# Kernel optimization log

Hardware: AMD Instinct MI355X
Metric: run time of the kernel (lower is better)

The kernel has to match this reference:

```python
import jax, jax.numpy as jnp
import numpy as np

GRID = 128
N = GRID * GRID  # number of torus nodes, node id v = x + GRID * y
HID = 64
OUT = 1
BATCH = 64


def _neighbor_idx():
    # Replicates gen_neighbor_lists: sparse matrices are permutation gathers
    # (A x)[v] = x[neighbor(v)] on a periodic grid.
    idx = np.arange(N)
    xc = idx % GRID
    yc = idx // GRID
    up = xc + ((yc + 1) % GRID) * GRID
    down = xc + ((yc - 1) % GRID) * GRID
    left = (xc - 1) % GRID + yc * GRID
    right = (xc + 1) % GRID + yc * GRID
    return np.stack([up, down, left, right], axis=0).astype(np.int32)  # [4, N]

NBR = jnp.asarray(_neighbor_idx())


def setup_inputs() -> dict:
    key = jax.random.key(0)
    ks = jax.random.split(key, 7)
    s4, sh = 1.0 / np.sqrt(4.0), 1.0 / np.sqrt(HID)
    return {
        "x": jax.random.normal(ks[0], (BATCH, N, 2), dtype=jnp.float32),
        "H": jnp.eye(2, dtype=jnp.float32),
        "W_emb": jax.random.uniform(ks[1], (4, HID), jnp.float32, -s4, s4),
        "b_emb": jax.random.uniform(ks[2], (HID,), jnp.float32, -s4, s4),
        "W_hid": jax.random.uniform(ks[3], (HID, HID), jnp.float32, -sh, sh),
        "b_hid": jax.random.uniform(ks[4], (HID,), jnp.float32, -sh, sh),
        "W_post": jax.random.uniform(ks[5], (HID, OUT), jnp.float32, -sh, sh),
        "b_post": jax.random.uniform(ks[6], (OUT,), jnp.float32, -sh, sh),
    }


def reference(x, H, W_emb, b_emb, W_hid, b_hid, W_post, b_post):
    # Permutation-matrix sparse.mm == direct neighbor gather: [B, 4, N, 2]
    xn = x[:, NBR, :]
    # Bilinear form per direction/node: s[b,i,k] = sum_{m,n} x[b,i,m] H[m,n] xn[b,k,i,n]
    s = jnp.einsum('bim,bkin,mn->bik', x, xn, H)  # [B, N, 4]
    h = jax.nn.relu(s @ W_emb + b_emb)            # [B, N, HID]
    h = jax.nn.relu(h @ W_hid + b_hid)            # [B, N, HID]
    h = h @ W_post + b_post                       # [B, N, OUT]
    return h.sum(axis=1)                          # [B, OUT]
```

## Files before the change

### kernel.cpp

```cpp
#include <hip/hip_runtime.h>
#include <hip/hip_bf16.h>

#define GRID_D 128
#define NSITES (GRID_D * GRID_D)
#define HID 64
#define BATCH 64

#define WPB 4
#define BLOCKS 1024
#define BLOCKS_PER_BATCH (BLOCKS / BATCH)
#define WAVES_PER_BATCH (BLOCKS_PER_BATCH * WPB)
#define SITES_PER_WAVE (NSITES / WAVES_PER_BATCH)
#define ITERS (SITES_PER_WAVE / 64)

typedef short bf16x8 __attribute__((ext_vector_type(8)));
typedef float f32x4  __attribute__((ext_vector_type(4)));

__device__ __forceinline__ unsigned short f2bf(float f) {
    return __builtin_bit_cast(unsigned short, __float2bfloat16(f));
}

__device__ __forceinline__ unsigned cvt_pk_bf16(float a, float b) {
    unsigned r;
    asm("v_cvt_pk_bf16_f32 %0, %1, %2" : "=v"(r) : "v"(a), "v"(b));
    return r;
}

union frag_u { bf16x8 v; unsigned u[4]; unsigned short us[8]; };

__global__ __launch_bounds__(256)
void gauge_mfma(const float* __restrict__ x,
                const float* __restrict__ H,
                const float* __restrict__ W_emb,
                const float* __restrict__ b_emb,
                const float* __restrict__ W_hid,
                const float* __restrict__ b_hid,
                const float* __restrict__ W_post,
                float* __restrict__ ws)
{
    const int tid   = threadIdx.x;
    const int lane  = tid & 63;
    const int widx  = tid >> 6;
    const int wgid  = blockIdx.x * WPB + widx;
    const int b     = wgid / WAVES_PER_BATCH;
    const int wslot = wgid % WAVES_PER_BATCH;

    const int  ls  = lane & 15;
    const int  kg  = lane >> 4;
    const bool kg0 = (kg == 0);

    const float h00 = H[0], h01 = H[1], h10 = H[2], h11 = H[3];

    bf16x8 bfrag[4][2];
    #pragma unroll
    for (int t = 0; t < 4; ++t) {
        #pragma unroll
        for (int s = 0; s < 2; ++s) {
            frag_u r;
            #pragma unroll
            for (int j = 0; j < 4; ++j) {
                const int i    = 2 * j;
                const int khid = s * 32 + ((i & 4) << 2) + (kg << 2) + (i & 3);
                r.u[j] = cvt_pk_bf16(W_hid[khid * HID + t * 16 + ls],
                                     W_hid[(khid + 1) * HID + t * 16 + ls]);
            }
            bfrag[t][s] = r.v;
        }
    }

    bf16x8 afe[4];
    #pragma unroll
    for (int m = 0; m < 4; ++m) {
        const int col = m * 16 + ls;
        frag_u r;
        r.u[0] = kg0 ? cvt_pk_bf16(W_emb[0 * HID + col], W_emb[1 * HID + col]) : 0u;
        r.u[1] = kg0 ? cvt_pk_bf16(W_emb[2 * HID + col], W_emb[3 * HID + col]) : 0u;
        r.u[2] = kg0 ? (unsigned)f2bf(b_emb[col]) : 0u;
        r.u[3] = 0u;
        afe[m] = r.v;
    }

    float bh[4], wp[4];
    #pragma unroll
    for (int t = 0; t < 4; ++t) {
        bh[t] = b_hid[t * 16 + ls];
        wp[t] = W_post[t * 16 + ls];
    }

    const float* __restrict__ xb = x + (size_t)b * NSITES * 2;
    const int wbase = wslot * SITES_PER_WAVE;
    const unsigned sd2 = kg0 ? 0x00003F80u : 0u;
    float o0 = 0.f, o1 = 0.f, o2 = 0.f, o3 = 0.f;

    for (int it = 0; it < ITERS; ++it) {
        const int site = wbase + it * 64 + lane;
        const int xc = site & (GRID_D - 1);
        const int yc = site >> 7;
        const int n0 = xc + (((yc + 1) & (GRID_D - 1)) << 7);
        const int n1 = xc + (((yc - 1) & (GRID_D - 1)) << 7);
        const int n2 = ((xc - 1) & (GRID_D - 1)) + (yc << 7);
        const int n3 = ((xc + 1) & (GRID_D - 1)) + (yc << 7);

        const float2 xi = *(const float2*)(xb + 2 * site);
        const float2 xu = *(const float2*)(xb + 2 * n0);
        const float2 xd = *(const float2*)(xb + 2 * n1);
        const float2 xl = *(const float2*)(xb + 2 * n2);
        const float2 xr = *(const float2*)(xb + 2 * n3);

        const float s0 = xi.x * fmaf(h00, xu.x, h01 * xu.y) + xi.y * fmaf(h10, xu.x, h11 * xu.y);
        const float s1 = xi.x * fmaf(h00, xd.x, h01 * xd.y) + xi.y * fmaf(h10, xd.x, h11 * xd.y);
        const float s2 = xi.x * fmaf(h00, xl.x, h01 * xl.y) + xi.y * fmaf(h10, xl.x, h11 * xl.y);
        const float s3 = xi.x * fmaf(h00, xr.x, h01 * xr.y) + xi.y * fmaf(h10, xr.x, h11 * xr.y);

        const unsigned p01 = cvt_pk_bf16(s0, s1);
        const unsigned p23 = cvt_pk_bf16(s2, s3);

        #pragma unroll
        for (int g = 0; g < 4; ++g) {
            const unsigned q0 = __shfl(p01, (g << 4) + ls, 64);
            const unsigned q1 = __shfl(p23, (g << 4) + ls, 64);
            frag_u bs;
            bs.u[0] = kg0 ? q0 : 0u;
            bs.u[1] = kg0 ? q1 : 0u;
            bs.u[2] = sd2;
            bs.u[3] = 0u;

            f32x4 D0 = {0.f, 0.f, 0.f, 0.f};
            f32x4 D1 = {0.f, 0.f, 0.f, 0.f};
            f32x4 D2 = {0.f, 0.f, 0.f, 0.f};
            f32x4 D3 = {0.f, 0.f, 0.f, 0.f};
            D0 = __builtin_amdgcn_mfma_f32_16x16x32_bf16(afe[0], bs.v, D0, 0, 0, 0);
            D1 = __builtin_amdgcn_mfma_f32_16x16x32_bf16(afe[1], bs.v, D1, 0, 0, 0);
            D2 = __builtin_amdgcn_mfma_f32_16x16x32_bf16(afe[2], bs.v, D2, 0, 0, 0);
            D3 = __builtin_amdgcn_mfma_f32_16x16x32_bf16(afe[3], bs.v, D3, 0, 0, 0);

            #pragma unroll
            for (int r = 0; r < 4; ++r) {
                D0[r] = fmaxf(D0[r], 0.0f);
                D1[r] = fmaxf(D1[r], 0.0f);
                D2[r] = fmaxf(D2[r], 0.0f);
                D3[r] = fmaxf(D3[r], 0.0f);
            }
            frag_u ah0, ah1;
            ah0.u[0] = cvt_pk_bf16(D0[0], D0[1]);
            ah0.u[1] = cvt_pk_bf16(D0[2], D0[3]);
            ah0.u[2] = cvt_pk_bf16(D1[0], D1[1]);
            ah0.u[3] = cvt_pk_bf16(D1[2], D1[3]);
            ah1.u[0] = cvt_pk_bf16(D2[0], D2[1]);
            ah1.u[1] = cvt_pk_bf16(D2[2], D2[3]);
            ah1.u[2] = cvt_pk_bf16(D3[0], D3[1]);
            ah1.u[3] = cvt_pk_bf16(D3[2], D3[3]);

            {
                f32x4 acc = { bh[0], bh[0], bh[0], bh[0] };
                acc = __builtin_amdgcn_mfma_f32_16x16x32_bf16(ah0.v, bfrag[0][0], acc, 0, 0, 0);
                acc = __builtin_amdgcn_mfma_f32_16x16x32_bf16(ah1.v, bfrag[0][1], acc, 0, 0, 0);
                #pragma unroll
                for (int r = 0; r < 4; ++r) o0 = fmaf(fmaxf(acc[r], 0.0f), wp[0], o0);
            }
            {
                f32x4 acc = { bh[1], bh[1], bh[1], bh[1] };
                acc = __builtin_amdgcn_mfma_f32_16x16x32_bf16(ah0.v, bfrag[1][0], acc, 0, 0, 0);
                acc = __builtin_amdgcn_mfma_f32_16x16x32_bf16(ah1.v, bfrag[1][1], acc, 0, 0, 0);
                #pragma unroll
                for (int r = 0; r < 4; ++r) o1 = fmaf(fmaxf(acc[r], 0.0f), wp[1], o1);
            }
            {
                f32x4 acc = { bh[2], bh[2], bh[2], bh[2] };
                acc = __builtin_amdgcn_mfma_f32_16x16x32_bf16(ah0.v, bfrag[2][0], acc, 0, 0, 0);
                acc = __builtin_amdgcn_mfma_f32_16x16x32_bf16(ah1.v, bfrag[2][1], acc, 0, 0, 0);
                #pragma unroll
                for (int r = 0; r < 4; ++r) o2 = fmaf(fmaxf(acc[r], 0.0f), wp[2], o2);
            }
            {
                f32x4 acc = { bh[3], bh[3], bh[3], bh[3] };
                acc = __builtin_amdgcn_mfma_f32_16x16x32_bf16(ah0.v, bfrag[3][0], acc, 0, 0, 0);
                acc = __builtin_amdgcn_mfma_f32_16x16x32_bf16(ah1.v, bfrag[3][1], acc, 0, 0, 0);
                #pragma unroll
                for (int r = 0; r < 4; ++r) o3 = fmaf(fmaxf(acc[r], 0.0f), wp[3], o3);
            }
        }
    }

    float o = (o0 + o1) + (o2 + o3);

    #pragma unroll
    for (int off = 32; off > 0; off >>= 1)
        o += __shfl_down(o, off, 64);

    __shared__ float part[WPB];
    if (lane == 0) part[widx] = o;
    __syncthreads();
    if (tid == 0)
        ws[blockIdx.x] = part[0] + part[1] + part[2] + part[3];
}

__global__ __launch_bounds__(64)
void gauge_reduce(const float* __restrict__ ws,
                  const float* __restrict__ b_post,
                  float* __restrict__ out)
{
    const int b = threadIdx.x;
    float t = (float)NSITES * b_post[0];
    #pragma unroll
    for (int j = 0; j < BLOCKS_PER_BATCH; ++j)
        t += ws[b * BLOCKS_PER_BATCH + j];
    out[b] = t;
}

extern "C" void kernel_launch(void* const* d_in, const int* in_sizes, int n_in,
                              void* d_out, int out_size, void* d_ws, size_t ws_size,
                              hipStream_t stream)
{
    const float* x      = (const float*)d_in[0];
    const float* H      = (const float*)d_in[1];
    const float* W_emb  = (const float*)d_in[2];
    const float* b_emb  = (const float*)d_in[3];
    const float* W_hid  = (const float*)d_in[4];
    const float* b_hid  = (const float*)d_in[5];
    const float* W_post = (const float*)d_in[6];
    const float* b_post = (const float*)d_in[7];
    float* out = (float*)d_out;
    float* ws  = (float*)d_ws;

    gauge_mfma<<<dim3(BLOCKS), dim3(256), 0, stream>>>(
        x, H, W_emb, b_emb, W_hid, b_hid, W_post, ws);
    gauge_reduce<<<dim3(1), dim3(64), 0, stream>>>(ws, b_post, out);
}
```

Baseline: 92.89 us.

## Prefetch next iteration's bilinear inputs and fold reduction into atomics

```diff
diff --git a/kernel.cpp b/kernel.cpp
--- a/kernel.cpp
+++ b/kernel.cpp
@@ -36,7 +36,8 @@
                 const float* __restrict__ W_hid,
                 const float* __restrict__ b_hid,
                 const float* __restrict__ W_post,
-                float* __restrict__ ws)
+                const float* __restrict__ b_post,
+                float* __restrict__ out)
 {
     const int tid   = threadIdx.x;
     const int lane  = tid & 63;
@@ -92,7 +93,7 @@
     const unsigned sd2 = kg0 ? 0x00003F80u : 0u;
     float o0 = 0.f, o1 = 0.f, o2 = 0.f, o3 = 0.f;
 
-    for (int it = 0; it < ITERS; ++it) {
+    auto s_phase = [&](int it, unsigned& p01, unsigned& p23) {
         const int site = wbase + it * 64 + lane;
         const int xc = site & (GRID_D - 1);
         const int yc = site >> 7;
@@ -100,25 +101,30 @@
         const int n1 = xc + (((yc - 1) & (GRID_D - 1)) << 7);
         const int n2 = ((xc - 1) & (GRID_D - 1)) + (yc << 7);
         const int n3 = ((xc + 1) & (GRID_D - 1)) + (yc << 7);
-
         const float2 xi = *(const float2*)(xb + 2 * site);
         const float2 xu = *(const float2*)(xb + 2 * n0);
         const float2 xd = *(const float2*)(xb + 2 * n1);
         const float2 xl = *(const float2*)(xb + 2 * n2);
         const float2 xr = *(const float2*)(xb + 2 * n3);
-
         const float s0 = xi.x * fmaf(h00, xu.x, h01 * xu.y) + xi.y * fmaf(h10, xu.x, h11 * xu.y);
         const float s1 = xi.x * fmaf(h00, xd.x, h01 * xd.y) + xi.y * fmaf(h10, xd.x, h11 * xd.y);
         const float s2 = xi.x * fmaf(h00, xl.x, h01 * xl.y) + xi.y * fmaf(h10, xl.x, h11 * xl.y);
         const float s3 = xi.x * fmaf(h00, xr.x, h01 * xr.y) + xi.y * fmaf(h10, xr.x, h11 * xr.y);
-
-        const unsigned p01 = cvt_pk_bf16(s0, s1);
-        const unsigned p23 = cvt_pk_bf16(s2, s3);
+        p01 = cvt_pk_bf16(s0, s1);
+        p23 = cvt_pk_bf16(s2, s3);
+    };
+
+    unsigned p01c, p23c, p01n, p23n;
+    s_phase(0, p01c, p23c);
+
+    for (int it = 0; it < ITERS; ++it) {
+        if (it + 1 < ITERS)
+            s_phase(it + 1, p01n, p23n);
 
         #pragma unroll
         for (int g = 0; g < 4; ++g) {
-            const unsigned q0 = __shfl(p01, (g << 4) + ls, 64);
-            const unsigned q1 = __shfl(p23, (g << 4) + ls, 64);
+            const unsigned q0 = __shfl(p01c, (g << 4) + ls, 64);
+            const unsigned q1 = __shfl(p23c, (g << 4) + ls, 64);
             frag_u bs;
             bs.u[0] = kg0 ? q0 : 0u;
             bs.u[1] = kg0 ? q1 : 0u;
@@ -180,6 +186,7 @@
                 for (int r = 0; r < 4; ++r) o3 = fmaf(fmaxf(acc[r], 0.0f), wp[3], o3);
             }
         }
+        p01c = p01n; p23c = p23n;
     }
 
     float o = (o0 + o1) + (o2 + o3);
@@ -191,21 +198,12 @@
     __shared__ float part[WPB];
     if (lane == 0) part[widx] = o;
     __syncthreads();
-    if (tid == 0)
-        ws[blockIdx.x] = part[0] + part[1] + part[2] + part[3];
-}
-
-__global__ __launch_bounds__(64)
-void gauge_reduce(const float* __restrict__ ws,
-                  const float* __restrict__ b_post,
-                  float* __restrict__ out)
-{
-    const int b = threadIdx.x;
-    float t = (float)NSITES * b_post[0];
-    #pragma unroll
-    for (int j = 0; j < BLOCKS_PER_BATCH; ++j)
-        t += ws[b * BLOCKS_PER_BATCH + j];
-    out[b] = t;
+    if (tid == 0) {
+        float t = part[0] + part[1] + part[2] + part[3];
+        if ((blockIdx.x % BLOCKS_PER_BATCH) == 0)
+            t += (float)NSITES * b_post[0];
+        atomicAdd(&out[b], t);
+    }
 }
 
 extern "C" void kernel_launch(void* const* d_in, const int* in_sizes, int n_in,
@@ -221,9 +219,9 @@
     const float* W_post = (const float*)d_in[6];
     const float* b_post = (const float*)d_in[7];
     float* out = (float*)d_out;
-    float* ws  = (float*)d_ws;
+
+    hipMemsetAsync(out, 0, (size_t)out_size * sizeof(float), stream);
 
     gauge_mfma<<<dim3(BLOCKS), dim3(256), 0, stream>>>(
-        x, H, W_emb, b_emb, W_hid, b_hid, W_post, ws);
-    gauge_reduce<<<dim3(1), dim3(64), 0, stream>>>(ws, b_post, out);
-}
+        x, H, W_emb, b_emb, W_hid, b_hid, W_post, b_post, out);
+}
```

Result: no change. 94.52 us (+1.8%).
